# Kernel optimization log

Measured on AMD Instinct MI355X. Metric: run time of the kernel, lower is better.

Reference implementation:

```python
import jax, jax.numpy as jnp
import numpy as np

B, C, CI, T, H, W = 2, 1024, 512, 32, 14, 14
N = T * H * W


def setup_inputs() -> dict:
    key = jax.random.key(0)
    ks = jax.random.split(key, 6)
    s_in = 1.0 / np.sqrt(C)
    s_mid = 1.0 / np.sqrt(CI)
    return {
        "x": jax.random.normal(ks[0], (B, C, T, H, W), jnp.float32),
        "Wk": jax.random.normal(ks[1], (CI, C), jnp.float32) * s_in,
        "bk": jnp.zeros((CI,), jnp.float32),
        "Wq": jax.random.normal(ks[2], (CI, C), jnp.float32) * s_in,
        "bq": jnp.zeros((CI,), jnp.float32),
        "Wv": jax.random.normal(ks[3], (CI, C), jnp.float32) * s_in,
        "bv": jnp.zeros((CI,), jnp.float32),
        "Wo": jax.random.normal(ks[4], (C, CI), jnp.float32) * s_mid,
        "bo": jnp.zeros((C,), jnp.float32),
    }


def reference(x, Wk, bk, Wq, bq, Wv, bv, Wo, bo):
    # x: (B, C, T, H, W). Dropout layers are identity at inference.
    b, c, t, h, w = x.shape
    n = t * h * w
    xf = x.reshape(b, c, n)                          # (B, C, N)
    k = jnp.einsum("dc,bcn->bdn", Wk, xf) + bk[None, :, None]   # (B, CI, N)
    q = jnp.einsum("dc,bcn->bdn", Wq, xf) + bq[None, :, None]   # (B, CI, N)
    v = jnp.einsum("dc,bcn->bdn", Wv, xf) + bv[None, :, None]   # (B, CI, N)
    # alpha[b,i,j] = sum_d key[b,i,d] * query[b,d,j], scaled by 1/T
    alpha = jnp.einsum("bdi,bdj->bij", k, q) / float(t)          # (B, N, N)
    alpha = jax.nn.softmax(alpha, axis=-1)
    # y (B, CI, N) with y[b,c,i] = sum_j alpha[b,i,j] * v[b,c,j]
    y = jnp.einsum("bij,bcj->bci", alpha, v)
    out = jnp.einsum("dc,bcn->bdn", Wo, y) + bo[None, :, None]   # (B, C, N)
    return out.reshape(b, c, t, h, w) + x
```

## Files before the change

kernel.cpp:

```cpp
#include <hip/hip_runtime.h>

#define Bb 2
#define Cc 1024
#define CIi 512
#define Nn 6272
#define JH 3136
#define SCALE (1.0f / 32.0f)

typedef __bf16 bf16;
typedef __bf16 bf16x8 __attribute__((ext_vector_type(8)));
typedef float f32x4 __attribute__((ext_vector_type(4)));
typedef unsigned int u32;
typedef unsigned char u8;
typedef unsigned int u32x4 __attribute__((ext_vector_type(4)));

__device__ __forceinline__ void g2l16(const void* g, void* l) {
  __builtin_amdgcn_global_load_lds(
      (const __attribute__((address_space(1))) u32*)g,
      (__attribute__((address_space(3))) u32*)(size_t)l, 16, 0, 0);
}

__device__ __forceinline__ u8 to_fp8(float v) {
  return (u8)(__builtin_amdgcn_cvt_pk_fp8_f32(v, v, 0, 0) & 0xff);
}

__global__ __launch_bounds__(256) void xpose_kernel(const float* __restrict__ x,
                                                    bf16* __restrict__ xT) {
  __shared__ float tile[32][33];
  int b = blockIdx.z;
  int n0 = blockIdx.x * 32, c0 = blockIdx.y * 32;
  int tn = threadIdx.x & 31, tr = threadIdx.x >> 5;
  const float* xp = x + ((size_t)b * Cc + c0) * Nn + n0;
  for (int i = 0; i < 4; i++) {
    int c = tr + i * 8;
    tile[c][tn] = xp[(size_t)c * Nn + tn];
  }
  __syncthreads();
  bf16* op = xT + ((size_t)b * Nn + n0) * Cc + c0;
  for (int i = 0; i < 4; i++) {
    int n = tr + i * 8;
    op[(size_t)n * Cc + tn] = (bf16)tile[tn][n];
  }
}

__global__ __launch_bounds__(256) void proj_kernel(
    const bf16* __restrict__ xT, const float* __restrict__ Wk,
    const float* __restrict__ Wq, const float* __restrict__ Wv,
    const float* __restrict__ bk, const float* __restrict__ bq,
    const float* __restrict__ bv, u8* __restrict__ kT8, u8* __restrict__ qT8,
    bf16* __restrict__ vv) {
  int z = blockIdx.z;
  int b = z / 3, proj = z % 3;
  const float* W = proj == 0 ? Wk : (proj == 1 ? Wq : Wv);
  const float* bias = proj == 0 ? bk : (proj == 1 ? bq : bv);
  int m0 = blockIdx.x * 128;
  int d0 = blockIdx.y * 128;
  __shared__ __align__(16) bf16 la[2][128 * 40];
  __shared__ __align__(16) bf16 lb[2][128 * 40];
  int tid = threadIdx.x;
  int wave = tid >> 6, lane = tid & 63, quad = lane >> 4, l16 = lane & 15;
  int wm = (wave >> 1) * 64, wn = (wave & 1) * 64;
  int row2 = tid >> 1, half = tid & 1;

  f32x4 acc[4][4] = {};
  const bf16* aSrc = xT + ((size_t)b * Nn + m0 + row2) * Cc + half * 16;
  const float* bSrc = W + (size_t)(d0 + row2) * Cc + half * 16;

  u32x4 a0, a1;
  f32x4 w0, w1, w2, w3;
  {
    const u32x4* ga = (const u32x4*)aSrc;
    a0 = ga[0];
    a1 = ga[1];
    const f32x4* gb = (const f32x4*)bSrc;
    w0 = gb[0]; w1 = gb[1]; w2 = gb[2]; w3 = gb[3];
  }
  {
    *(u32x4*)&la[0][row2 * 40 + half * 16] = a0;
    *(u32x4*)&la[0][row2 * 40 + half * 16 + 8] = a1;
    bf16x8 p0 = {(bf16)w0[0], (bf16)w0[1], (bf16)w0[2], (bf16)w0[3],
                 (bf16)w1[0], (bf16)w1[1], (bf16)w1[2], (bf16)w1[3]};
    bf16x8 p1 = {(bf16)w2[0], (bf16)w2[1], (bf16)w2[2], (bf16)w2[3],
                 (bf16)w3[0], (bf16)w3[1], (bf16)w3[2], (bf16)w3[3]};
    *(bf16x8*)&lb[0][row2 * 40 + half * 16] = p0;
    *(bf16x8*)&lb[0][row2 * 40 + half * 16 + 8] = p1;
  }
  __syncthreads();

  const int NSTEP = Cc / 32;
  for (int step = 0; step < NSTEP; step++) {
    int cur = step & 1;
    if (step + 1 < NSTEP) {
      const u32x4* ga = (const u32x4*)(aSrc + (step + 1) * 32);
      a0 = ga[0];
      a1 = ga[1];
      const f32x4* gb = (const f32x4*)(bSrc + (step + 1) * 32);
      w0 = gb[0]; w1 = gb[1]; w2 = gb[2]; w3 = gb[3];
    }
    bf16x8 af[4], bfr[4];
#pragma unroll
    for (int t = 0; t < 4; t++)
      af[t] = *(const bf16x8*)&la[cur][(wm + t * 16 + l16) * 40 + quad * 8];
#pragma unroll
    for (int t = 0; t < 4; t++)
      bfr[t] = *(const bf16x8*)&lb[cur][(wn + t * 16 + l16) * 40 + quad * 8];
#pragma unroll
    for (int tm = 0; tm < 4; tm++)
#pragma unroll
      for (int tn = 0; tn < 4; tn++)
        acc[tm][tn] = __builtin_amdgcn_mfma_f32_16x16x32_bf16(
            af[tm], bfr[tn], acc[tm][tn], 0, 0, 0);
    if (step + 1 < NSTEP) {
      *(u32x4*)&la[cur ^ 1][row2 * 40 + half * 16] = a0;
      *(u32x4*)&la[cur ^ 1][row2 * 40 + half * 16 + 8] = a1;
      bf16x8 p0 = {(bf16)w0[0], (bf16)w0[1], (bf16)w0[2], (bf16)w0[3],
                   (bf16)w1[0], (bf16)w1[1], (bf16)w1[2], (bf16)w1[3]};
      bf16x8 p1 = {(bf16)w2[0], (bf16)w2[1], (bf16)w2[2], (bf16)w2[3],
                   (bf16)w3[0], (bf16)w3[1], (bf16)w3[2], (bf16)w3[3]};
      *(bf16x8*)&lb[cur ^ 1][row2 * 40 + half * 16] = p0;
      *(bf16x8*)&lb[cur ^ 1][row2 * 40 + half * 16 + 8] = p1;
      __syncthreads();
    }
  }
  for (int tn = 0; tn < 4; tn++) {
    int dcol = d0 + wn + tn * 16 + l16;
    float bval = bias[dcol];
    for (int tm = 0; tm < 4; tm++) {
      int nbase = m0 + wm + tm * 16 + quad * 4;
      for (int r = 0; r < 4; r++) {
        float val = acc[tm][tn][r] + bval;
        int nrow = nbase + r;
        if (proj == 0) {
          kT8[((size_t)b * Nn + nrow) * CIi + dcol] = to_fp8(val);
        } else if (proj == 1) {
          int ch = (dcol >> 3) ^ (nrow & 15);
          qT8[((size_t)b * Nn + nrow) * CIi + ch * 8 + (dcol & 7)] =
              to_fp8(val);
        } else {
          vv[((size_t)b * CIi + dcol) * Nn + nrow] = (bf16)val;
        }
      }
    }
  }
}

__global__ __launch_bounds__(512, 2) void attn_kernel(
    const u8* __restrict__ kT8, const u8* __restrict__ qT8,
    const bf16* __restrict__ vv, bf16* __restrict__ yp,
    float* __restrict__ ml) {
  int l = blockIdx.x;
  int jh = l & 1, b = (l >> 1) & 1;
  int i0 = (l >> 2) * 128;
  int tid = threadIdx.x;
  int wave = tid >> 6, lane = tid & 63, quad = lane >> 4, l16 = lane & 15;
  int dw = wave * 64;

  __shared__ __align__(16) u8 lq[2][64 * 512];
  __shared__ __align__(16) bf16 Psm[128 * 72];
  __shared__ float redi[128];

  const u8* qb = qT8 + ((size_t)b * Nn + (size_t)jh * JH) * CIi;
  const bf16* vb = vv + (size_t)b * CIi * Nn + (size_t)jh * JH;

  long kf[16];
  {
    const u8* kp = kT8 + ((size_t)b * Nn + i0 + wave * 16 + l16) * CIi +
                   quad * 8;
#pragma unroll
    for (int kk = 0; kk < 16; kk++)
      kf[kk] = *(const long*)(kp + kk * 32);
  }
  f32x4 oacc[8][4] = {};
  f32x4 l_acc = {};

  {
    const u8* qrow = qb + (size_t)(wave * 8) * CIi + lane * 16;
#pragma unroll
    for (int r = 0; r < 4; r++)
      g2l16(qrow + r * 1024, &lq[0][(wave * 8) * 512 + r * 1024]);
  }
  __syncthreads();

  for (int j0 = 0; j0 < JH; j0 += 64) {
    int t = (j0 >> 6) & 1;
    u32x4 vf[2][4];
#pragma unroll
    for (int jc = 0; jc < 2; jc++)
#pragma unroll
      for (int ds = 0; ds < 4; ds++)
        vf[jc][ds] = *(const u32x4*)(vb + (size_t)(dw + ds * 16 + l16) * Nn +
                                     j0 + jc * 32 + quad * 8);
    __builtin_amdgcn_sched_barrier(0);
    if (j0 + 64 < JH) {
      const u8* qrow = qb + (size_t)(j0 + 64 + wave * 8) * CIi + lane * 16;
#pragma unroll
      for (int r = 0; r < 4; r++)
        g2l16(qrow + r * 1024, &lq[t ^ 1][(wave * 8) * 512 + r * 1024]);
    }
    f32x4 s[4] = {};
    {
      const u8* q0 = &lq[t][l16 * 512];
#pragma unroll
      for (int kk = 0; kk < 16; kk++) {
        int sl = ((kk * 4 + quad) ^ l16) * 8;
        long qf0 = *(const long*)(q0 + sl);
        long qf1 = *(const long*)(q0 + 16 * 512 + sl);
        long qf2 = *(const long*)(q0 + 32 * 512 + sl);
        long qf3 = *(const long*)(q0 + 48 * 512 + sl);
        s[0] = __builtin_amdgcn_mfma_f32_16x16x32_fp8_fp8(kf[kk], qf0, s[0],
                                                          0, 0, 0);
        s[1] = __builtin_amdgcn_mfma_f32_16x16x32_fp8_fp8(kf[kk], qf1, s[1],
                                                          0, 0, 0);
        s[2] = __builtin_amdgcn_mfma_f32_16x16x32_fp8_fp8(kf[kk], qf2, s[2],
                                                          0, 0, 0);
        s[3] = __builtin_amdgcn_mfma_f32_16x16x32_fp8_fp8(kf[kk], qf3, s[3],
                                                          0, 0, 0);
      }
    }
    {
#pragma unroll
      for (int jb = 0; jb < 4; jb++)
#pragma unroll
        for (int r = 0; r < 4; r++) {
          float p = __expf(fminf(fmaf(s[jb][r], SCALE, -2.0f), 20.0f));
          l_acc[r] += p;
          int gi = wave * 16 + quad * 4 + r;
          int gj = jb * 16 + l16;
          Psm[gi * 72 + gj] = (bf16)p;
        }
    }
    asm volatile("s_waitcnt lgkmcnt(0)" ::: "memory");
    __builtin_amdgcn_s_barrier();
    asm volatile("" ::: "memory");

#pragma unroll
    for (int jc = 0; jc < 2; jc++)
#pragma unroll
      for (int is = 0; is < 8; is++) {
        bf16x8 pf = *(const bf16x8*)&Psm[(is * 16 + l16) * 72 + jc * 32 +
                                         quad * 8];
#pragma unroll
        for (int ds = 0; ds < 4; ds++)
          oacc[is][ds] = __builtin_amdgcn_mfma_f32_16x16x32_bf16(
              pf, __builtin_bit_cast(bf16x8, vf[jc][ds]), oacc[is][ds], 0, 0,
              0);
      }
    __syncthreads();
  }

#pragma unroll
  for (int o = 1; o < 16; o <<= 1)
#pragma unroll
    for (int r = 0; r < 4; r++) l_acc[r] += __shfl_xor(l_acc[r], o);
  if (l16 == 0) {
#pragma unroll
    for (int r = 0; r < 4; r++) {
      int gi = wave * 16 + quad * 4 + r;
      ml[(size_t)(jh * Bb + b) * Nn + i0 + gi] = l_acc[r];
      redi[gi] = 1.0f / l_acc[r];
    }
  }
  __syncthreads();
  bf16* ypb = yp + ((size_t)jh * Bb + b) * Nn * CIi;
#pragma unroll
  for (int is = 0; is < 8; is++) {
    f32x4 inv = *(const f32x4*)&redi[is * 16 + quad * 4];
#pragma unroll
    for (int ds = 0; ds < 4; ds++)
#pragma unroll
      for (int r = 0; r < 4; r++)
        ypb[(size_t)(i0 + is * 16 + quad * 4 + r) * CIi + dw + ds * 16 + l16] =
            (bf16)(oacc[is][ds][r] * inv[r]);
  }
}

__global__ __launch_bounds__(256) void merge_kernel(const bf16* __restrict__ yp,
                                                    const float* __restrict__ ml,
                                                    bf16* __restrict__ y) {
  int idx = blockIdx.x * 256 + threadIdx.x;
  int row = idx >> 6, c = idx & 63;
  float l0 = ml[row];
  float l1 = ml[(size_t)Bb * Nn + row];
  float inv = 1.0f / (l0 + l1);
  float w0 = l0 * inv, w1 = l1 * inv;
  bf16x8 v0 = *(const bf16x8*)&yp[(size_t)row * CIi + c * 8];
  bf16x8 v1 =
      *(const bf16x8*)&yp[(size_t)Bb * Nn * CIi + (size_t)row * CIi + c * 8];
  bf16x8 o;
#pragma unroll
  for (int k = 0; k < 8; k++)
    o[k] = (bf16)(w0 * (float)v0[k] + w1 * (float)v1[k]);
  *(bf16x8*)&y[(size_t)row * CIi + c * 8] = o;
}

__global__ __launch_bounds__(256) void out_kernel(
    const bf16* __restrict__ y, const float* __restrict__ Wo,
    const float* __restrict__ bo, const float* __restrict__ x,
    float* __restrict__ out) {
  int b = blockIdx.z;
  int d0 = blockIdx.x * 128;
  int m0 = blockIdx.y * 128;
  __shared__ __align__(16) bf16 la[2][128 * 40];
  __shared__ __align__(16) bf16 lb[2][128 * 40];
  int tid = threadIdx.x;
  int wave = tid >> 6, lane = tid & 63, quad = lane >> 4, l16 = lane & 15;
  int wm = (wave >> 1) * 64, wn = (wave & 1) * 64;
  int row2 = tid >> 1, half = tid & 1;
  f32x4 acc[4][4] = {};
  const float* aSrc = Wo + (size_t)(d0 + row2) * CIi + half * 16;
  const bf16* bSrc = y + ((size_t)b * Nn + m0 + row2) * CIi + half * 16;

  f32x4 w0, w1, w2, w3;
  u32x4 b0, b1;
  {
    const f32x4* ga = (const f32x4*)aSrc;
    w0 = ga[0]; w1 = ga[1]; w2 = ga[2]; w3 = ga[3];
    const u32x4* gb = (const u32x4*)bSrc;
    b0 = gb[0];
    b1 = gb[1];
  }
  {
    bf16x8 p0 = {(bf16)w0[0], (bf16)w0[1], (bf16)w0[2], (bf16)w0[3],
                 (bf16)w1[0], (bf16)w1[1], (bf16)w1[2], (bf16)w1[3]};
    bf16x8 p1 = {(bf16)w2[0], (bf16)w2[1], (bf16)w2[2], (bf16)w2[3],
                 (bf16)w3[0], (bf16)w3[1], (bf16)w3[2], (bf16)w3[3]};
    *(bf16x8*)&la[0][row2 * 40 + half * 16] = p0;
    *(bf16x8*)&la[0][row2 * 40 + half * 16 + 8] = p1;
    *(u32x4*)&lb[0][row2 * 40 + half * 16] = b0;
    *(u32x4*)&lb[0][row2 * 40 + half * 16 + 8] = b1;
  }
  __syncthreads();

  const int NSTEP = CIi / 32;
  for (int step = 0; step < NSTEP; step++) {
    int cur = step & 1;
    if (step + 1 < NSTEP) {
      const f32x4* ga = (const f32x4*)(aSrc + (step + 1) * 32);
      w0 = ga[0]; w1 = ga[1]; w2 = ga[2]; w3 = ga[3];
      const u32x4* gb = (const u32x4*)(bSrc + (step + 1) * 32);
      b0 = gb[0];
      b1 = gb[1];
    }
    bf16x8 af[4], bfr[4];
#pragma unroll
    for (int t = 0; t < 4; t++)
      af[t] = *(const bf16x8*)&la[cur][(wm + t * 16 + l16) * 40 + quad * 8];
#pragma unroll
    for (int t = 0; t < 4; t++)
      bfr[t] = *(const bf16x8*)&lb[cur][(wn + t * 16 + l16) * 40 + quad * 8];
#pragma unroll
    for (int tm = 0; tm < 4; tm++)
#pragma unroll
      for (int tn = 0; tn < 4; tn++)
        acc[tm][tn] = __builtin_amdgcn_mfma_f32_16x16x32_bf16(
            af[tm], bfr[tn], acc[tm][tn], 0, 0, 0);
    if (step + 1 < NSTEP) {
      bf16x8 p0 = {(bf16)w0[0], (bf16)w0[1], (bf16)w0[2], (bf16)w0[3],
                   (bf16)w1[0], (bf16)w1[1], (bf16)w1[2], (bf16)w1[3]};
      bf16x8 p1 = {(bf16)w2[0], (bf16)w2[1], (bf16)w2[2], (bf16)w2[3],
                   (bf16)w3[0], (bf16)w3[1], (bf16)w3[2], (bf16)w3[3]};
      *(bf16x8*)&la[cur ^ 1][row2 * 40 + half * 16] = p0;
      *(bf16x8*)&la[cur ^ 1][row2 * 40 + half * 16 + 8] = p1;
      *(u32x4*)&lb[cur ^ 1][row2 * 40 + half * 16] = b0;
      *(u32x4*)&lb[cur ^ 1][row2 * 40 + half * 16 + 8] = b1;
      __syncthreads();
    }
  }
  for (int tm = 0; tm < 4; tm++) {
    for (int r = 0; r < 4; r++) {
      int drow = d0 + wm + tm * 16 + quad * 4 + r;
      float bval = bo[drow];
      const float* xrow = x + ((size_t)b * Cc + drow) * Nn;
      float* orow = out + ((size_t)b * Cc + drow) * Nn;
      for (int tn = 0; tn < 4; tn++) {
        int ncol = m0 + wn + tn * 16 + l16;
        orow[ncol] = acc[tm][tn][r] + bval + xrow[ncol];
      }
    }
  }
}

extern "C" void kernel_launch(void* const* d_in, const int* in_sizes, int n_in,
                              void* d_out, int out_size, void* d_ws,
                              size_t ws_size, hipStream_t stream) {
  (void)in_sizes;
  (void)n_in;
  (void)out_size;
  (void)ws_size;
  const float* x = (const float*)d_in[0];
  const float* Wk = (const float*)d_in[1];
  const float* bk = (const float*)d_in[2];
  const float* Wq = (const float*)d_in[3];
  const float* bq = (const float*)d_in[4];
  const float* Wv = (const float*)d_in[5];
  const float* bv = (const float*)d_in[6];
  const float* Wo = (const float*)d_in[7];
  const float* bo = (const float*)d_in[8];
  float* out = (float*)d_out;

  bf16* xT = (bf16*)d_ws;
  bf16* yp = (bf16*)d_ws;
  bf16* y = (bf16*)d_ws + (size_t)Bb * Nn * Cc;
  u8* kT8 = (u8*)d_out;
  u8* qT8 = kT8 + (size_t)Bb * Nn * CIi;
  bf16* vv = (bf16*)(qT8 + (size_t)Bb * Nn * CIi);
  float* ml = (float*)((char*)d_out + (size_t)40 * 1024 * 1024);

  xpose_kernel<<<dim3(Nn / 32, Cc / 32, Bb), 256, 0, stream>>>(x, xT);
  proj_kernel<<<dim3(Nn / 128, CIi / 128, 3 * Bb), 256, 0, stream>>>(
      xT, Wk, Wq, Wv, bk, bq, bv, kT8, qT8, vv);
  attn_kernel<<<dim3((Nn / 128) * 2 * Bb), 512, 0, stream>>>(kT8, qT8, vv, yp,
                                                             ml);
  merge_kernel<<<dim3(Bb * Nn * 64 / 256), 256, 0, stream>>>(yp, ml, y);
  out_kernel<<<dim3(Cc / 128, Nn / 128, Bb), 256, 0, stream>>>(y, Wo, bo, x,
                                                               out);
}
```

Before: 483.9 us.

## Deepen register prefetch in projection GEMMs and stage V output through LDS

The proj and out GEMM kernels now keep two K-steps of global loads in flight in registers, unrolling the main loop by two with fixed LDS buffers so that load latency has more compute to hide behind. The proj kernel's V output, previously written as scattered 2-byte stores along the N dimension, is first transposed into shared memory and then written with contiguous 16-byte vector stores. The trade-off is higher register pressure from the doubled prefetch registers, which may reduce occupancy, and an extra LDS round trip plus barriers in the epilogue.

```diff
diff --git a/kernel.cpp b/kernel.cpp
--- a/kernel.cpp
+++ b/kernel.cpp
@@ -55,8 +55,9 @@
   const float* bias = proj == 0 ? bk : (proj == 1 ? bq : bv);
   int m0 = blockIdx.x * 128;
   int d0 = blockIdx.y * 128;
-  __shared__ __align__(16) bf16 la[2][128 * 40];
-  __shared__ __align__(16) bf16 lb[2][128 * 40];
+  __shared__ __align__(16) bf16 smem[4 * 128 * 40];
+  bf16* la[2] = {smem, smem + 128 * 40};
+  bf16* lb[2] = {smem + 2 * 128 * 40, smem + 3 * 128 * 40};
   int tid = threadIdx.x;
   int wave = tid >> 6, lane = tid & 63, quad = lane >> 4, l16 = lane & 15;
   int wm = (wave >> 1) * 64, wn = (wave & 1) * 64;
@@ -66,78 +67,133 @@
   const bf16* aSrc = xT + ((size_t)b * Nn + m0 + row2) * Cc + half * 16;
   const float* bSrc = W + (size_t)(d0 + row2) * Cc + half * 16;
 
-  u32x4 a0, a1;
-  f32x4 w0, w1, w2, w3;
+  u32x4 aA0, aA1, aB0, aB1;
+  f32x4 wA0, wA1, wA2, wA3, wB0, wB1, wB2, wB3;
   {
     const u32x4* ga = (const u32x4*)aSrc;
-    a0 = ga[0];
-    a1 = ga[1];
+    aA0 = ga[0]; aA1 = ga[1];
     const f32x4* gb = (const f32x4*)bSrc;
-    w0 = gb[0]; w1 = gb[1]; w2 = gb[2]; w3 = gb[3];
+    wA0 = gb[0]; wA1 = gb[1]; wA2 = gb[2]; wA3 = gb[3];
+    const u32x4* ga2 = (const u32x4*)(aSrc + 32);
+    aB0 = ga2[0]; aB1 = ga2[1];
+    const f32x4* gb2 = (const f32x4*)(bSrc + 32);
+    wB0 = gb2[0]; wB1 = gb2[1]; wB2 = gb2[2]; wB3 = gb2[3];
   }
   {
-    *(u32x4*)&la[0][row2 * 40 + half * 16] = a0;
-    *(u32x4*)&la[0][row2 * 40 + half * 16 + 8] = a1;
-    bf16x8 p0 = {(bf16)w0[0], (bf16)w0[1], (bf16)w0[2], (bf16)w0[3],
-                 (bf16)w1[0], (bf16)w1[1], (bf16)w1[2], (bf16)w1[3]};
-    bf16x8 p1 = {(bf16)w2[0], (bf16)w2[1], (bf16)w2[2], (bf16)w2[3],
-                 (bf16)w3[0], (bf16)w3[1], (bf16)w3[2], (bf16)w3[3]};
+    *(u32x4*)&la[0][row2 * 40 + half * 16] = aA0;
+    *(u32x4*)&la[0][row2 * 40 + half * 16 + 8] = aA1;
+    bf16x8 p0 = {(bf16)wA0[0], (bf16)wA0[1], (bf16)wA0[2], (bf16)wA0[3],
+                 (bf16)wA1[0], (bf16)wA1[1], (bf16)wA1[2], (bf16)wA1[3]};
+    bf16x8 p1 = {(bf16)wA2[0], (bf16)wA2[1], (bf16)wA2[2], (bf16)wA2[3],
+                 (bf16)wA3[0], (bf16)wA3[1], (bf16)wA3[2], (bf16)wA3[3]};
     *(bf16x8*)&lb[0][row2 * 40 + half * 16] = p0;
     *(bf16x8*)&lb[0][row2 * 40 + half * 16 + 8] = p1;
   }
   __syncthreads();
 
   const int NSTEP = Cc / 32;
-  for (int step = 0; step < NSTEP; step++) {
-    int cur = step & 1;
-    if (step + 1 < NSTEP) {
-      const u32x4* ga = (const u32x4*)(aSrc + (step + 1) * 32);
-      a0 = ga[0];
-      a1 = ga[1];
-      const f32x4* gb = (const f32x4*)(bSrc + (step + 1) * 32);
-      w0 = gb[0]; w1 = gb[1]; w2 = gb[2]; w3 = gb[3];
-    }
-    bf16x8 af[4], bfr[4];
-#pragma unroll
-    for (int t = 0; t < 4; t++)
-      af[t] = *(const bf16x8*)&la[cur][(wm + t * 16 + l16) * 40 + quad * 8];
-#pragma unroll
-    for (int t = 0; t < 4; t++)
-      bfr[t] = *(const bf16x8*)&lb[cur][(wn + t * 16 + l16) * 40 + quad * 8];
-#pragma unroll
-    for (int tm = 0; tm < 4; tm++)
-#pragma unroll
-      for (int tn = 0; tn < 4; tn++)
-        acc[tm][tn] = __builtin_amdgcn_mfma_f32_16x16x32_bf16(
-            af[tm], bfr[tn], acc[tm][tn], 0, 0, 0);
-    if (step + 1 < NSTEP) {
-      *(u32x4*)&la[cur ^ 1][row2 * 40 + half * 16] = a0;
-      *(u32x4*)&la[cur ^ 1][row2 * 40 + half * 16 + 8] = a1;
-      bf16x8 p0 = {(bf16)w0[0], (bf16)w0[1], (bf16)w0[2], (bf16)w0[3],
-                   (bf16)w1[0], (bf16)w1[1], (bf16)w1[2], (bf16)w1[3]};
-      bf16x8 p1 = {(bf16)w2[0], (bf16)w2[1], (bf16)w2[2], (bf16)w2[3],
-                   (bf16)w3[0], (bf16)w3[1], (bf16)w3[2], (bf16)w3[3]};
-      *(bf16x8*)&lb[cur ^ 1][row2 * 40 + half * 16] = p0;
-      *(bf16x8*)&lb[cur ^ 1][row2 * 40 + half * 16 + 8] = p1;
+  for (int k = 0; k < NSTEP; k += 2) {
+    if (k + 2 < NSTEP) {
+      const u32x4* ga = (const u32x4*)(aSrc + (k + 2) * 32);
+      aA0 = ga[0]; aA1 = ga[1];
+      const f32x4* gb = (const f32x4*)(bSrc + (k + 2) * 32);
+      wA0 = gb[0]; wA1 = gb[1]; wA2 = gb[2]; wA3 = gb[3];
+    }
+    {
+      bf16x8 af[4], bfr[4];
+#pragma unroll
+      for (int t = 0; t < 4; t++)
+        af[t] = *(const bf16x8*)&la[0][(wm + t * 16 + l16) * 40 + quad * 8];
+#pragma unroll
+      for (int t = 0; t < 4; t++)
+        bfr[t] = *(const bf16x8*)&lb[0][(wn + t * 16 + l16) * 40 + quad * 8];
+#pragma unroll
+      for (int tm = 0; tm < 4; tm++)
+#pragma unroll
+        for (int tn = 0; tn < 4; tn++)
+          acc[tm][tn] = __builtin_amdgcn_mfma_f32_16x16x32_bf16(
+              af[tm], bfr[tn], acc[tm][tn], 0, 0, 0);
+    }
+    {
+      *(u32x4*)&la[1][row2 * 40 + half * 16] = aB0;
+      *(u32x4*)&la[1][row2 * 40 + half * 16 + 8] = aB1;
+      bf16x8 p0 = {(bf16)wB0[0], (bf16)wB0[1], (bf16)wB0[2], (bf16)wB0[3],
+                   (bf16)wB1[0], (bf16)wB1[1], (bf16)wB1[2], (bf16)wB1[3]};
+      bf16x8 p1 = {(bf16)wB2[0], (bf16)wB2[1], (bf16)wB2[2], (bf16)wB2[3],
+                   (bf16)wB3[0], (bf16)wB3[1], (bf16)wB3[2], (bf16)wB3[3]};
+      *(bf16x8*)&lb[1][row2 * 40 + half * 16] = p0;
+      *(bf16x8*)&lb[1][row2 * 40 + half * 16 + 8] = p1;
+    }
+    __syncthreads();
+    if (k + 3 < NSTEP) {
+      const u32x4* ga = (const u32x4*)(aSrc + (k + 3) * 32);
+      aB0 = ga[0]; aB1 = ga[1];
+      const f32x4* gb = (const f32x4*)(bSrc + (k + 3) * 32);
+      wB0 = gb[0]; wB1 = gb[1]; wB2 = gb[2]; wB3 = gb[3];
+    }
+    {
+      bf16x8 af[4], bfr[4];
+#pragma unroll
+      for (int t = 0; t < 4; t++)
+        af[t] = *(const bf16x8*)&la[1][(wm + t * 16 + l16) * 40 + quad * 8];
+#pragma unroll
+      for (int t = 0; t < 4; t++)
+        bfr[t] = *(const bf16x8*)&lb[1][(wn + t * 16 + l16) * 40 + quad * 8];
+#pragma unroll
+      for (int tm = 0; tm < 4; tm++)
+#pragma unroll
+        for (int tn = 0; tn < 4; tn++)
+          acc[tm][tn] = __builtin_amdgcn_mfma_f32_16x16x32_bf16(
+              af[tm], bfr[tn], acc[tm][tn], 0, 0, 0);
+    }
+    if (k + 2 < NSTEP) {
+      *(u32x4*)&la[0][row2 * 40 + half * 16] = aA0;
+      *(u32x4*)&la[0][row2 * 40 + half * 16 + 8] = aA1;
+      bf16x8 p0 = {(bf16)wA0[0], (bf16)wA0[1], (bf16)wA0[2], (bf16)wA0[3],
+                   (bf16)wA1[0], (bf16)wA1[1], (bf16)wA1[2], (bf16)wA1[3]};
+      bf16x8 p1 = {(bf16)wA2[0], (bf16)wA2[1], (bf16)wA2[2], (bf16)wA2[3],
+                   (bf16)wA3[0], (bf16)wA3[1], (bf16)wA3[2], (bf16)wA3[3]};
+      *(bf16x8*)&lb[0][row2 * 40 + half * 16] = p0;
+      *(bf16x8*)&lb[0][row2 * 40 + half * 16 + 8] = p1;
       __syncthreads();
     }
   }
-  for (int tn = 0; tn < 4; tn++) {
-    int dcol = d0 + wn + tn * 16 + l16;
-    float bval = bias[dcol];
-    for (int tm = 0; tm < 4; tm++) {
-      int nbase = m0 + wm + tm * 16 + quad * 4;
-      for (int r = 0; r < 4; r++) {
-        float val = acc[tm][tn][r] + bval;
-        int nrow = nbase + r;
-        if (proj == 0) {
-          kT8[((size_t)b * Nn + nrow) * CIi + dcol] = to_fp8(val);
-        } else if (proj == 1) {
-          int ch = (dcol >> 3) ^ (nrow & 15);
-          qT8[((size_t)b * Nn + nrow) * CIi + ch * 8 + (dcol & 7)] =
-              to_fp8(val);
-        } else {
-          vv[((size_t)b * CIi + dcol) * Nn + nrow] = (bf16)val;
+
+  __syncthreads();
+  if (proj == 2) {
+    bf16* vt = smem;
+    for (int tn = 0; tn < 4; tn++) {
+      int dl = wn + tn * 16 + l16;
+      float bval = bias[d0 + dl];
+      for (int tm = 0; tm < 4; tm++) {
+        int nb = wm + tm * 16 + quad * 4;
+        for (int r = 0; r < 4; r++)
+          vt[dl * 132 + nb + r] = (bf16)(acc[tm][tn][r] + bval);
+      }
+    }
+    __syncthreads();
+    int d = tid >> 1, nh = tid & 1;
+    bf16* dst = vv + ((size_t)b * CIi + d0 + d) * Nn + m0 + nh * 64;
+    const bf16* src = &vt[d * 132 + nh * 64];
+#pragma unroll
+    for (int i = 0; i < 8; i++)
+      *(bf16x8*)(dst + i * 8) = *(const bf16x8*)(src + i * 8);
+  } else {
+    for (int tn = 0; tn < 4; tn++) {
+      int dcol = d0 + wn + tn * 16 + l16;
+      float bval = bias[dcol];
+      for (int tm = 0; tm < 4; tm++) {
+        int nbase = m0 + wm + tm * 16 + quad * 4;
+        for (int r = 0; r < 4; r++) {
+          float val = acc[tm][tn][r] + bval;
+          int nrow = nbase + r;
+          if (proj == 0) {
+            kT8[((size_t)b * Nn + nrow) * CIi + dcol] = to_fp8(val);
+          } else {
+            int ch = (dcol >> 3) ^ (nrow & 15);
+            qT8[((size_t)b * Nn + nrow) * CIi + ch * 8 + (dcol & 7)] =
+                to_fp8(val);
+          }
         }
       }
     }
@@ -300,8 +356,9 @@
   int b = blockIdx.z;
   int d0 = blockIdx.x * 128;
   int m0 = blockIdx.y * 128;
-  __shared__ __align__(16) bf16 la[2][128 * 40];
-  __shared__ __align__(16) bf16 lb[2][128 * 40];
+  __shared__ __align__(16) bf16 smem[4 * 128 * 40];
+  bf16* la[2] = {smem, smem + 128 * 40};
+  bf16* lb[2] = {smem + 2 * 128 * 40, smem + 3 * 128 * 40};
   int tid = threadIdx.x;
   int wave = tid >> 6, lane = tid & 63, quad = lane >> 4, l16 = lane & 15;
   int wm = (wave >> 1) * 64, wn = (wave & 1) * 64;
@@ -310,59 +367,94 @@
   const float* aSrc = Wo + (size_t)(d0 + row2) * CIi + half * 16;
   const bf16* bSrc = y + ((size_t)b * Nn + m0 + row2) * CIi + half * 16;
 
-  f32x4 w0, w1, w2, w3;
-  u32x4 b0, b1;
+  f32x4 wA0, wA1, wA2, wA3, wB0, wB1, wB2, wB3;
+  u32x4 bA0, bA1, bB0, bB1;
   {
     const f32x4* ga = (const f32x4*)aSrc;
-    w0 = ga[0]; w1 = ga[1]; w2 = ga[2]; w3 = ga[3];
+    wA0 = ga[0]; wA1 = ga[1]; wA2 = ga[2]; wA3 = ga[3];
     const u32x4* gb = (const u32x4*)bSrc;
-    b0 = gb[0];
-    b1 = gb[1];
+    bA0 = gb[0]; bA1 = gb[1];
+    const f32x4* ga2 = (const f32x4*)(aSrc + 32);
+    wB0 = ga2[0]; wB1 = ga2[1]; wB2 = ga2[2]; wB3 = ga2[3];
+    const u32x4* gb2 = (const u32x4*)(bSrc + 32);
+    bB0 = gb2[0]; bB1 = gb2[1];
   }
   {
-    bf16x8 p0 = {(bf16)w0[0], (bf16)w0[1], (bf16)w0[2], (bf16)w0[3],
-                 (bf16)w1[0], (bf16)w1[1], (bf16)w1[2], (bf16)w1[3]};
-    bf16x8 p1 = {(bf16)w2[0], (bf16)w2[1], (bf16)w2[2], (bf16)w2[3],
-                 (bf16)w3[0], (bf16)w3[1], (bf16)w3[2], (bf16)w3[3]};
+    bf16x8 p0 = {(bf16)wA0[0], (bf16)wA0[1], (bf16)wA0[2], (bf16)wA0[3],
+                 (bf16)wA1[0], (bf16)wA1[1], (bf16)wA1[2], (bf16)wA1[3]};
+    bf16x8 p1 = {(bf16)wA2[0], (bf16)wA2[1], (bf16)wA2[2], (bf16)wA2[3],
+                 (bf16)wA3[0], (bf16)wA3[1], (bf16)wA3[2], (bf16)wA3[3]};
     *(bf16x8*)&la[0][row2 * 40 + half * 16] = p0;
     *(bf16x8*)&la[0][row2 * 40 + half * 16 + 8] = p1;
-    *(u32x4*)&lb[0][row2 * 40 + half * 16] = b0;
-    *(u32x4*)&lb[0][row2 * 40 + half * 16 + 8] = b1;
+    *(u32x4*)&lb[0][row2 * 40 + half * 16] = bA0;
+    *(u32x4*)&lb[0][row2 * 40 + half * 16 + 8] = bA1;
   }
   __syncthreads();
 
   const int NSTEP = CIi / 32;
-  for (int step = 0; step < NSTEP; step++) {
-    int cur = step & 1;
-    if (step + 1 < NSTEP) {
-      const f32x4* ga = (const f32x4*)(aSrc + (step + 1) * 32);
-      w0 = ga[0]; w1 = ga[1]; w2 = ga[2]; w3 = ga[3];
-      const u32x4* gb = (const u32x4*)(bSrc + (step + 1) * 32);
-      b0 = gb[0];
-      b1 = gb[1];
-    }
-    bf16x8 af[4], bfr[4];
-#pragma unroll
-    for (int t = 0; t < 4; t++)
-      af[t] = *(const bf16x8*)&la[cur][(wm + t * 16 + l16) * 40 + quad * 8];
-#pragma unroll
-    for (int t = 0; t < 4; t++)
-      bfr[t] = *(const bf16x8*)&lb[cur][(wn + t * 16 + l16) * 40 + quad * 8];
-#pragma unroll
-    for (int tm = 0; tm < 4; tm++)
-#pragma unroll
-      for (int tn = 0; tn < 4; tn++)
-        acc[tm][tn] = __builtin_amdgcn_mfma_f32_16x16x32_bf16(
-            af[tm], bfr[tn], acc[tm][tn], 0, 0, 0);
-    if (step + 1 < NSTEP) {
-      bf16x8 p0 = {(bf16)w0[0], (bf16)w0[1], (bf16)w0[2], (bf16)w0[3],
-                   (bf16)w1[0], (bf16)w1[1], (bf16)w1[2], (bf16)w1[3]};
-      bf16x8 p1 = {(bf16)w2[0], (bf16)w2[1], (bf16)w2[2], (bf16)w2[3],
-                   (bf16)w3[0], (bf16)w3[1], (bf16)w3[2], (bf16)w3[3]};
-      *(bf16x8*)&la[cur ^ 1][row2 * 40 + half * 16] = p0;
-      *(bf16x8*)&la[cur ^ 1][row2 * 40 + half * 16 + 8] = p1;
-      *(u32x4*)&lb[cur ^ 1][row2 * 40 + half * 16] = b0;
-      *(u32x4*)&lb[cur ^ 1][row2 * 40 + half * 16 + 8] = b1;
+  for (int k = 0; k < NSTEP; k += 2) {
+    if (k + 2 < NSTEP) {
+      const f32x4* ga = (const f32x4*)(aSrc + (k + 2) * 32);
+      wA0 = ga[0]; wA1 = ga[1]; wA2 = ga[2]; wA3 = ga[3];
+      const u32x4* gb = (const u32x4*)(bSrc + (k + 2) * 32);
+      bA0 = gb[0]; bA1 = gb[1];
+    }
+    {
+      bf16x8 af[4], bfr[4];
+#pragma unroll
+      for (int t = 0; t < 4; t++)
+        af[t] = *(const bf16x8*)&la[0][(wm + t * 16 + l16) * 40 + quad * 8];
+#pragma unroll
+      for (int t = 0; t < 4; t++)
+        bfr[t] = *(const bf16x8*)&lb[0][(wn + t * 16 + l16) * 40 + quad * 8];
+#pragma unroll
+      for (int tm = 0; tm < 4; tm++)
+#pragma unroll
+        for (int tn = 0; tn < 4; tn++)
+          acc[tm][tn] = __builtin_amdgcn_mfma_f32_16x16x32_bf16(
+              af[tm], bfr[tn], acc[tm][tn], 0, 0, 0);
+    }
+    {
+      bf16x8 p0 = {(bf16)wB0[0], (bf16)wB0[1], (bf16)wB0[2], (bf16)wB0[3],
+                   (bf16)wB1[0], (bf16)wB1[1], (bf16)wB1[2], (bf16)wB1[3]};
+      bf16x8 p1 = {(bf16)wB2[0], (bf16)wB2[1], (bf16)wB2[2], (bf16)wB2[3],
+                   (bf16)wB3[0], (bf16)wB3[1], (bf16)wB3[2], (bf16)wB3[3]};
+      *(bf16x8*)&la[1][row2 * 40 + half * 16] = p0;
+      *(bf16x8*)&la[1][row2 * 40 + half * 16 + 8] = p1;
+      *(u32x4*)&lb[1][row2 * 40 + half * 16] = bB0;
+      *(u32x4*)&lb[1][row2 * 40 + half * 16 + 8] = bB1;
+    }
+    __syncthreads();
+    if (k + 3 < NSTEP) {
+      const f32x4* ga = (const f32x4*)(aSrc + (k + 3) * 32);
+      wB0 = ga[0]; wB1 = ga[1]; wB2 = ga[2]; wB3 = ga[3];
+      const u32x4* gb = (const u32x4*)(bSrc + (k + 3) * 32);
+      bB0 = gb[0]; bB1 = gb[1];
+    }
+    {
+      bf16x8 af[4], bfr[4];
+#pragma unroll
+      for (int t = 0; t < 4; t++)
+        af[t] = *(const bf16x8*)&la[1][(wm + t * 16 + l16) * 40 + quad * 8];
+#pragma unroll
+      for (int t = 0; t < 4; t++)
+        bfr[t] = *(const bf16x8*)&lb[1][(wn + t * 16 + l16) * 40 + quad * 8];
+#pragma unroll
+      for (int tm = 0; tm < 4; tm++)
+#pragma unroll
+        for (int tn = 0; tn < 4; tn++)
+          acc[tm][tn] = __builtin_amdgcn_mfma_f32_16x16x32_bf16(
+              af[tm], bfr[tn], acc[tm][tn], 0, 0, 0);
+    }
+    if (k + 2 < NSTEP) {
+      bf16x8 p0 = {(bf16)wA0[0], (bf16)wA0[1], (bf16)wA0[2], (bf16)wA0[3],
+                   (bf16)wA1[0], (bf16)wA1[1], (bf16)wA1[2], (bf16)wA1[3]};
+      bf16x8 p1 = {(bf16)wA2[0], (bf16)wA2[1], (bf16)wA2[2], (bf16)wA2[3],
+                   (bf16)wA3[0], (bf16)wA3[1], (bf16)wA3[2], (bf16)wA3[3]};
+      *(bf16x8*)&la[0][row2 * 40 + half * 16] = p0;
+      *(bf16x8*)&la[0][row2 * 40 + half * 16 + 8] = p1;
+      *(u32x4*)&lb[0][row2 * 40 + half * 16] = bA0;
+      *(u32x4*)&lb[0][row2 * 40 + half * 16 + 8] = bA1;
       __syncthreads();
     }
   }
```

Result: slower. 500.7 us (+3.5%).

## Software-pipeline QK score tile with PV accumulation using double-buffered P

Applied to the files above, without the earlier changes.

Restructures the attention loop so that the QK^T MFMA and softmax-exp for tile k+1 run interleaved with the PV MFMA for tile k. P is double-buffered in shared memory and Q is prefetched two tiles ahead, which removes one barrier per iteration. The intent is to overlap the fp8 score MFMAs and exp work with the bf16 PV MFMAs. In exchange it uses more LDS and needs a prologue and epilogue, which may raise register pressure under launch_bounds(512,2).

```diff
diff --git a/kernel.cpp b/kernel.cpp
--- a/kernel.cpp
+++ b/kernel.cpp
@@ -5,6 +5,7 @@
 #define CIi 512
 #define Nn 6272
 #define JH 3136
+#define NT 49
 #define SCALE (1.0f / 32.0f)
 
 typedef __bf16 bf16;
@@ -156,7 +157,7 @@
   int dw = wave * 64;
 
   __shared__ __align__(16) u8 lq[2][64 * 512];
-  __shared__ __align__(16) bf16 Psm[128 * 72];
+  __shared__ __align__(16) bf16 Psm[2][128 * 72];
   __shared__ float redi[128];
 
   const u8* qb = qT8 + ((size_t)b * Nn + (size_t)jh * JH) * CIi;
@@ -178,28 +179,63 @@
 #pragma unroll
     for (int r = 0; r < 4; r++)
       g2l16(qrow + r * 1024, &lq[0][(wave * 8) * 512 + r * 1024]);
-  }
-  __syncthreads();
-
-  for (int j0 = 0; j0 < JH; j0 += 64) {
-    int t = (j0 >> 6) & 1;
+    const u8* qrow1 = qb + (size_t)(64 + wave * 8) * CIi + lane * 16;
+#pragma unroll
+    for (int r = 0; r < 4; r++)
+      g2l16(qrow1 + r * 1024, &lq[1][(wave * 8) * 512 + r * 1024]);
+  }
+  __syncthreads();
+
+  {
+    f32x4 s[4] = {};
+    const u8* q0 = &lq[0][l16 * 512];
+#pragma unroll
+    for (int kk = 0; kk < 16; kk++) {
+      int sl = ((kk * 4 + quad) ^ l16) * 8;
+      long qf0 = *(const long*)(q0 + sl);
+      long qf1 = *(const long*)(q0 + 16 * 512 + sl);
+      long qf2 = *(const long*)(q0 + 32 * 512 + sl);
+      long qf3 = *(const long*)(q0 + 48 * 512 + sl);
+      s[0] = __builtin_amdgcn_mfma_f32_16x16x32_fp8_fp8(kf[kk], qf0, s[0], 0,
+                                                        0, 0);
+      s[1] = __builtin_amdgcn_mfma_f32_16x16x32_fp8_fp8(kf[kk], qf1, s[1], 0,
+                                                        0, 0);
+      s[2] = __builtin_amdgcn_mfma_f32_16x16x32_fp8_fp8(kf[kk], qf2, s[2], 0,
+                                                        0, 0);
+      s[3] = __builtin_amdgcn_mfma_f32_16x16x32_fp8_fp8(kf[kk], qf3, s[3], 0,
+                                                        0, 0);
+    }
+#pragma unroll
+    for (int jb = 0; jb < 4; jb++)
+#pragma unroll
+      for (int r = 0; r < 4; r++) {
+        float p = __expf(fminf(fmaf(s[jb][r], SCALE, -2.0f), 20.0f));
+        l_acc[r] += p;
+        Psm[0][(wave * 16 + quad * 4 + r) * 72 + jb * 16 + l16] = (bf16)p;
+      }
+  }
+  __syncthreads();
+
+  for (int k = 0; k < NT; k++) {
+    int pb = k & 1;
     u32x4 vf[2][4];
 #pragma unroll
     for (int jc = 0; jc < 2; jc++)
 #pragma unroll
       for (int ds = 0; ds < 4; ds++)
         vf[jc][ds] = *(const u32x4*)(vb + (size_t)(dw + ds * 16 + l16) * Nn +
-                                     j0 + jc * 32 + quad * 8);
+                                     k * 64 + jc * 32 + quad * 8);
     __builtin_amdgcn_sched_barrier(0);
-    if (j0 + 64 < JH) {
-      const u8* qrow = qb + (size_t)(j0 + 64 + wave * 8) * CIi + lane * 16;
+    if (k + 2 < NT) {
+      const u8* qrow =
+          qb + (size_t)((k + 2) * 64 + wave * 8) * CIi + lane * 16;
 #pragma unroll
       for (int r = 0; r < 4; r++)
-        g2l16(qrow + r * 1024, &lq[t ^ 1][(wave * 8) * 512 + r * 1024]);
-    }
-    f32x4 s[4] = {};
-    {
-      const u8* q0 = &lq[t][l16 * 512];
+        g2l16(qrow + r * 1024, &lq[pb][(wave * 8) * 512 + r * 1024]);
+    }
+    if (k + 1 < NT) {
+      f32x4 s[4] = {};
+      const u8* q0 = &lq[pb ^ 1][l16 * 512];
 #pragma unroll
       for (int kk = 0; kk < 16; kk++) {
         int sl = ((kk * 4 + quad) ^ l16) * 8;
@@ -215,36 +251,38 @@
                                                           0, 0, 0);
         s[3] = __builtin_amdgcn_mfma_f32_16x16x32_fp8_fp8(kf[kk], qf3, s[3],
                                                           0, 0, 0);
-      }
-    }
-    {
-#pragma unroll
-      for (int jb = 0; jb < 4; jb++)
-#pragma unroll
-        for (int r = 0; r < 4; r++) {
-          float p = __expf(fminf(fmaf(s[jb][r], SCALE, -2.0f), 20.0f));
-          l_acc[r] += p;
-          int gi = wave * 16 + quad * 4 + r;
-          int gj = jb * 16 + l16;
-          Psm[gi * 72 + gj] = (bf16)p;
-        }
-    }
-    asm volatile("s_waitcnt lgkmcnt(0)" ::: "memory");
-    __builtin_amdgcn_s_barrier();
-    asm volatile("" ::: "memory");
-
-#pragma unroll
-    for (int jc = 0; jc < 2; jc++)
-#pragma unroll
-      for (int is = 0; is < 8; is++) {
-        bf16x8 pf = *(const bf16x8*)&Psm[(is * 16 + l16) * 72 + jc * 32 +
-                                         quad * 8];
+        int jc = kk >> 3, is = kk & 7;
+        bf16x8 pf = *(const bf16x8*)&Psm[pb][(is * 16 + l16) * 72 + jc * 32 +
+                                            quad * 8];
 #pragma unroll
         for (int ds = 0; ds < 4; ds++)
           oacc[is][ds] = __builtin_amdgcn_mfma_f32_16x16x32_bf16(
               pf, __builtin_bit_cast(bf16x8, vf[jc][ds]), oacc[is][ds], 0, 0,
               0);
       }
+#pragma unroll
+      for (int jb = 0; jb < 4; jb++)
+#pragma unroll
+        for (int r = 0; r < 4; r++) {
+          float p = __expf(fminf(fmaf(s[jb][r], SCALE, -2.0f), 20.0f));
+          l_acc[r] += p;
+          Psm[pb ^ 1][(wave * 16 + quad * 4 + r) * 72 + jb * 16 + l16] =
+              (bf16)p;
+        }
+    } else {
+#pragma unroll
+      for (int jc = 0; jc < 2; jc++)
+#pragma unroll
+        for (int is = 0; is < 8; is++) {
+          bf16x8 pf = *(const bf16x8*)&Psm[pb][(is * 16 + l16) * 72 +
+                                              jc * 32 + quad * 8];
+#pragma unroll
+          for (int ds = 0; ds < 4; ds++)
+            oacc[is][ds] = __builtin_amdgcn_mfma_f32_16x16x32_bf16(
+                pf, __builtin_bit_cast(bf16x8, vf[jc][ds]), oacc[is][ds], 0,
+                0, 0);
+        }
+    }
     __syncthreads();
   }
 
```

Measured after the change: 506.4 us. 1.05x slower.
